# Performance work log

Hardware: AMD Instinct MI355X
Metric: run time of the kernel (lower is better)

## Reference

```python
import jax, jax.numpy as jnp
import numpy as np

H = 8  # num_heads (init kwarg)

def setup_inputs() -> dict:
    key = jax.random.key(0)
    k1, k2, k3, k4 = jax.random.split(key, 4)
    B, S, E = 4, 2048, 512
    x = jax.random.normal(k1, (B, S, E), dtype=jnp.float32)
    # 'normal' keras initializer ~ N(0, 0.05)
    Wq = jax.random.normal(k2, (E, E), dtype=jnp.float32) * 0.05
    Wk = jax.random.normal(k3, (E, E), dtype=jnp.float32) * 0.05
    Wv = jax.random.normal(k4, (E, E), dtype=jnp.float32) * 0.05
    return {"x": x, "Wq": Wq, "Wk": Wk, "Wv": Wv}

def _split_heads(t):
    # [B,S,E] -> [H,B,S,E/H]; matches tf.stack(tf.split(t, H, axis=2))
    B, S, E = t.shape
    return t.reshape(B, S, H, E // H).transpose(2, 0, 1, 3)

def reference(x, Wq, Wk, Wv):
    B, S, E = x.shape
    q = _split_heads(jnp.einsum('bse,ef->bsf', x, Wq))  # [H,B,S,dh]
    k = _split_heads(jnp.einsum('bse,ef->bsf', x, Wk))
    v = _split_heads(jnp.einsum('bse,ef->bsf', x, Wv))
    # NOTE: original has NO 1/sqrt(d) scaling
    scores = jnp.einsum('hbqd,hbkd->hbqk', q, k)         # [H,B,S,S]
    attn = jax.nn.softmax(scores, axis=-1)
    effect = jnp.einsum('hbqk,hbkd->hbqd', attn, v)      # [H,B,S,dh]
    # tf.concat(tf.split(effect, H), axis=-1) + squeeze == merge heads on last dim
    out = effect.transpose(1, 2, 0, 3).reshape(B, S, E)  # [B,S,E]
    return (out, x)
```

## Files before the change

kernel.cpp:

```cpp
#include <hip/hip_runtime.h>

typedef _Float16 f16x8 __attribute__((ext_vector_type(8)));
typedef __fp16 h16x2 __attribute__((ext_vector_type(2)));
typedef float f32x4 __attribute__((ext_vector_type(4)));
typedef float f32x16 __attribute__((ext_vector_type(16)));

#define GF(r) ((((r)&3)) ^ (((r)>>2)&3))
#define LOG2E 1.44269504088896f

#define GLD16(gp, lp) __builtin_amdgcn_global_load_lds( \
    (const __attribute__((address_space(1))) void*)(gp), \
    (__attribute__((address_space(3))) void*)(lp), 16, 0, 0)

__global__ void cvt_all_kernel(const float4* __restrict__ x4, f16x8* __restrict__ xh,
                               const float* __restrict__ Wq, const float* __restrict__ Wk,
                               const float* __restrict__ Wv, _Float16* __restrict__ wt) {
    const int blk = blockIdx.x;
    const int tid = threadIdx.x;
    if (blk < 2048) {
        int i = blk * 256 + tid;
        float4 a = x4[2 * i], b = x4[2 * i + 1];
        f16x8 h;
        h[0] = (_Float16)a.x; h[1] = (_Float16)a.y; h[2] = (_Float16)a.z; h[3] = (_Float16)a.w;
        h[4] = (_Float16)b.x; h[5] = (_Float16)b.y; h[6] = (_Float16)b.z; h[7] = (_Float16)b.w;
        xh[i] = h;
    } else {
        __shared__ _Float16 lt[64 * 66];
        const int t = blk - 2048;
        const int mat = t >> 6, tile = t & 63;
        const int r0 = (tile >> 3) * 64, n0 = (tile & 7) * 64;
        const float* W = (mat == 0) ? Wq : ((mat == 1) ? Wk : Wv);
        const int rr = tid >> 4, c4 = tid & 15;
#pragma unroll
        for (int i = 0; i < 4; ++i) {
            int row = rr + i * 16;
            float4 v = *(const float4*)&W[(size_t)(r0 + row) * 512 + n0 + c4 * 4];
            lt[(c4 * 4 + 0) * 66 + row] = (_Float16)v.x;
            lt[(c4 * 4 + 1) * 66 + row] = (_Float16)v.y;
            lt[(c4 * 4 + 2) * 66 + row] = (_Float16)v.z;
            lt[(c4 * 4 + 3) * 66 + row] = (_Float16)v.w;
        }
        __syncthreads();
        const int nl = tid >> 2, rc = tid & 3;
        _Float16* dst = wt + (size_t)mat * 262144 + (size_t)(n0 + nl) * 512 + r0 + rc * 16;
#pragma unroll
        for (int u = 0; u < 2; ++u)
            *(f16x8*)(dst + u * 8) = *(const f16x8*)&lt[nl * 66 + rc * 16 + u * 8];
    }
}

__global__ __launch_bounds__(256, 3) void gemm_qkv(
    const _Float16* __restrict__ xh, const _Float16* __restrict__ wt,
    _Float16* __restrict__ qh, _Float16* __restrict__ kh, _Float16* __restrict__ vt) {
    __shared__ __align__(16) char gsm[49152];
    const int bid = blockIdx.x;
    const int xcdid = bid & 7, slot = bid >> 3;
    const int mtile = xcdid * 8 + (slot / 12);
    const int rem = slot % 12;
    const int mat = rem >> 2, ntile = rem & 3;
    const _Float16* wp = wt + (size_t)mat * 262144;
    const int tid = threadIdx.x, lane = tid & 63;
    const int g = lane >> 4, c = lane & 15;
    const int wid = tid >> 6, wm = wid >> 1, wn = wid & 1;

    f32x4 acc[4][4];
#pragma unroll
    for (int i = 0; i < 4; ++i)
#pragma unroll
        for (int j = 0; j < 4; ++j) acc[i][j] = (f32x4){0.f, 0.f, 0.f, 0.f};

    const int row0 = tid >> 2, p0 = tid & 3;

    auto GSTAGE = [&](int buf, int ks) {
        _Float16* la_ = (_Float16*)(gsm + buf * 16384);
        _Float16* lb_ = (_Float16*)(gsm + buf * 16384 + 8192);
        int r = row0, pp = p0 ^ GF(r);
        GLD16(xh + (size_t)(mtile * 128 + r) * 512 + ks * 32 + pp * 8, &la_[tid * 8]);
        GLD16(wp + (size_t)(ntile * 128 + r) * 512 + ks * 32 + pp * 8, &lb_[tid * 8]);
        r = 64 + row0; pp = p0 ^ GF(r);
        GLD16(xh + (size_t)(mtile * 128 + r) * 512 + ks * 32 + pp * 8, &la_[(256 + tid) * 8]);
        GLD16(wp + (size_t)(ntile * 128 + r) * 512 + ks * 32 + pp * 8, &lb_[(256 + tid) * 8]);
    };

    auto GTILE = [&](int ks) {
        const _Float16* la = (const _Float16*)(gsm + (ks % 3) * 16384);
        const _Float16* lb = (const _Float16*)(gsm + (ks % 3) * 16384 + 8192);
        f16x8 af[4], bf[4];
#pragma unroll
        for (int i = 0; i < 4; ++i) {
            int ra = wm * 64 + i * 16 + c;
            af[i] = *(const f16x8*)&la[ra * 32 + ((g ^ GF(ra)) * 8)];
            int rb = wn * 64 + i * 16 + c;
            bf[i] = *(const f16x8*)&lb[rb * 32 + ((g ^ GF(rb)) * 8)];
        }
        __builtin_amdgcn_s_setprio(1);
#pragma unroll
        for (int mi = 0; mi < 4; ++mi)
#pragma unroll
            for (int ni = 0; ni < 4; ++ni)
                acc[mi][ni] = __builtin_amdgcn_mfma_f32_16x16x32_f16(af[mi], bf[ni], acc[mi][ni], 0, 0, 0);
        __builtin_amdgcn_s_setprio(0);
    };

    GSTAGE(0, 0); GSTAGE(1, 1);
#pragma unroll 1
    for (int ks = 0; ks < 14; ++ks) {
        asm volatile("s_waitcnt vmcnt(4)" ::: "memory");
        __builtin_amdgcn_s_barrier();
        __builtin_amdgcn_sched_barrier(0);
        GSTAGE((ks + 2) % 3, ks + 2);
        GTILE(ks);
    }
    asm volatile("s_waitcnt vmcnt(4)" ::: "memory");
    __builtin_amdgcn_s_barrier();
    GTILE(14);
    asm volatile("s_waitcnt vmcnt(0)" ::: "memory");
    __builtin_amdgcn_s_barrier();
    GTILE(15);

    __syncthreads();
    _Float16* eb = (_Float16*)gsm + wid * 4608;
    const int rr = lane >> 3, cc = lane & 7;

    if (mat < 2) {
#pragma unroll
        for (int mi = 0; mi < 4; ++mi)
#pragma unroll
            for (int ni = 0; ni < 4; ++ni)
#pragma unroll
                for (int r = 0; r < 4; ++r)
                    eb[(mi * 16 + g * 4 + r) * 72 + ni * 16 + c] = (_Float16)acc[mi][ni][r];
        asm volatile("s_waitcnt lgkmcnt(0)" ::: "memory");
        _Float16* dstm = (mat == 0 ? qh : kh);
#pragma unroll
        for (int p = 0; p < 8; ++p) {
            int row = p * 8 + rr;
            f16x8 v = *(const f16x8*)&eb[row * 72 + cc * 8];
            *(f16x8*)(dstm + (size_t)(mtile * 128 + wm * 64 + row) * 512 +
                      ntile * 128 + wn * 64 + cc * 8) = v;
        }
    } else {
#pragma unroll
        for (int mi = 0; mi < 4; ++mi)
#pragma unroll
            for (int ni = 0; ni < 4; ++ni)
#pragma unroll
                for (int r = 0; r < 4; ++r)
                    eb[(ni * 16 + c) * 72 + mi * 16 + g * 4 + r] = (_Float16)acc[mi][ni][r];
        asm volatile("s_waitcnt lgkmcnt(0)" ::: "memory");
        const int h = ntile * 2 + wn;
        const int mbase = mtile * 128 + wm * 64;
        const int b = mbase >> 11, s0 = mbase & 2047;
#pragma unroll
        for (int p = 0; p < 8; ++p) {
            int d = p * 8 + rr;
            f16x8 v = *(const f16x8*)&eb[d * 72 + cc * 8];
            *(f16x8*)(vt + (((size_t)h * 4 + b) * 64 + d) * 2048 + s0 + cc * 8) = v;
        }
    }
}

__global__ __launch_bounds__(512, 4) void attn_kernel(
    const _Float16* __restrict__ qh, const _Float16* __restrict__ kh,
    const _Float16* __restrict__ vt, const float4* __restrict__ x4,
    float* __restrict__ out) {
    __shared__ __align__(16) char smem[65536];

    const int bid = blockIdx.x;
    const int xcd = bid & 7, idx = bid >> 3;
    const int hb = xcd * 4 + (idx >> 4);
    const int qblk = idx & 15;
    const int h = hb >> 2, b = hb & 3;
    const int tid = threadIdx.x, lane = tid & 63, wid = tid >> 6;
    const int qg = wid & 3, half = wid >> 2;
    const int q = lane & 31, hi = lane >> 5;

    {
        float4* xd = (float4*)(out + 4194304) + (size_t)bid * 2048;
        const float4* xs = x4 + (size_t)bid * 2048;
#pragma unroll
        for (int i = 0; i < 4; ++i) xd[i * 512 + tid] = xs[i * 512 + tid];
    }

    const int qrow0 = qblk * 128 + qg * 32;
    const _Float16* qp = qh + ((size_t)b * 2048 + qrow0) * 512 + h * 64;
    const _Float16* kp = kh + (size_t)b * 2048 * 512 + h * 64;
    const _Float16* vp = vt + (size_t)hb * 64 * 2048;

    const int srow = tid >> 3;
    const int ssw = (tid & 7) ^ ((srow ^ (srow >> 3)) & 7);

    auto STAGE = [&](int i) {
        char* base = smem + (i & 1) * 32768;
        GLD16(kp + ((size_t)(i * 64 + srow) * 512) + ssw * 8, (_Float16*)(base) + tid * 8);
        GLD16(vp + (size_t)srow * 2048 + i * 64 + ssw * 8, (_Float16*)(base + 8192) + tid * 8);
        GLD16(kp + ((size_t)((16 + i) * 64 + srow) * 512) + ssw * 8, (_Float16*)(base + 16384) + tid * 8);
        GLD16(vp + (size_t)srow * 2048 + (16 + i) * 64 + ssw * 8, (_Float16*)(base + 24576) + tid * 8);
    };

    f16x8 aQ[4];
#pragma unroll
    for (int kc = 0; kc < 4; ++kc)
        aQ[kc] = *(const f16x8*)(qp + (size_t)q * 512 + kc * 16 + hi * 8);

    float mrow = -1e30f, lrow = 0.f;
    f32x16 o0, o1;
#pragma unroll
    for (int i = 0; i < 16; ++i) { o0[i] = 0.f; o1[i] = 0.f; }

    const h16x2 ONE2 = {(__fp16)1.0f, (__fp16)1.0f};
    const int swr0 = (q ^ (q >> 3)) & 7;
    const int swr1 = ((32 + q) ^ ((32 + q) >> 3)) & 7;

    auto KPTR = [&](int t) {
        return (const _Float16*)(smem + (t & 1) * 32768 + half * 16384);
    };

    auto QKT2 = [&](const _Float16* kb, f32x16& s0, f32x16& s1) {
        f32x16 z0, z1;
#pragma unroll
        for (int i = 0; i < 16; ++i) { z0[i] = 0.f; z1[i] = 0.f; }
        __builtin_amdgcn_s_setprio(1);
#pragma unroll
        for (int kc = 0; kc < 4; ++kc) {
            f16x8 ak0 = *(const f16x8*)&kb[q * 64 + (((2 * kc + hi) ^ swr0) * 8)];
            f16x8 ak1 = *(const f16x8*)&kb[(32 + q) * 64 + (((2 * kc + hi) ^ swr1) * 8)];
            z0 = __builtin_amdgcn_mfma_f32_32x32x16_f16(ak0, aQ[kc], z0, 0, 0, 0);
            z1 = __builtin_amdgcn_mfma_f32_32x32x16_f16(ak1, aQ[kc], z1, 0, 0, 0);
        }
        __builtin_amdgcn_s_setprio(0);
        s0 = z0; s1 = z1;
    };

    auto SMPV2 = [&](f32x16& s0, f32x16& s1, const _Float16* vb) {
        float pm;
        {
            float m0 = fmaxf(fmaxf(fmaxf(s0[0], s0[1]), s0[2]), s0[3]);
            float m1 = fmaxf(fmaxf(fmaxf(s0[4], s0[5]), s0[6]), s0[7]);
            float m2 = fmaxf(fmaxf(fmaxf(s0[8], s0[9]), s0[10]), s0[11]);
            float m3 = fmaxf(fmaxf(fmaxf(s0[12], s0[13]), s0[14]), s0[15]);
            float m4 = fmaxf(fmaxf(fmaxf(s1[0], s1[1]), s1[2]), s1[3]);
            float m5 = fmaxf(fmaxf(fmaxf(s1[4], s1[5]), s1[6]), s1[7]);
            float m6 = fmaxf(fmaxf(fmaxf(s1[8], s1[9]), s1[10]), s1[11]);
            float m7 = fmaxf(fmaxf(fmaxf(s1[12], s1[13]), s1[14]), s1[15]);
            float t0 = fmaxf(fmaxf(m0, m1), m2);
            float t1 = fmaxf(fmaxf(m3, m4), m5);
            float t2 = fmaxf(m6, m7);
            pm = fmaxf(fmaxf(t0, t1), t2);
        }
        pm = fmaxf(pm, __shfl_xor(pm, 32));
        if (__any(pm > mrow + 8.0f)) {
            const float nm = fmaxf(mrow, pm);
            const float e = __builtin_amdgcn_exp2f((mrow - nm) * LOG2E);
            mrow = nm;
            lrow *= e;
            o0 *= e;
            o1 *= e;
        }
        const float nm2 = mrow * LOG2E;

#pragma unroll
        for (int i = 0; i < 16; ++i)
            s0[i] = __builtin_amdgcn_exp2f(fmaf(s0[i], LOG2E, -nm2));
#pragma unroll
        for (int i = 0; i < 16; ++i)
            s1[i] = __builtin_amdgcn_exp2f(fmaf(s1[i], LOG2E, -nm2));

        f16x8 pf[4];
        float rsA = 0.f, rsB = 0.f;
#pragma unroll
        for (int kb2 = 0; kb2 < 2; ++kb2) {
            const f32x16& sv = kb2 ? s1 : s0;
            h16x2 p0 = __builtin_amdgcn_cvt_pkrtz(sv[0], sv[1]);
            h16x2 p1 = __builtin_amdgcn_cvt_pkrtz(sv[2], sv[3]);
            h16x2 p2 = __builtin_amdgcn_cvt_pkrtz(sv[4], sv[5]);
            h16x2 p3 = __builtin_amdgcn_cvt_pkrtz(sv[6], sv[7]);
            h16x2 p4 = __builtin_amdgcn_cvt_pkrtz(sv[8], sv[9]);
            h16x2 p5 = __builtin_amdgcn_cvt_pkrtz(sv[10], sv[11]);
            h16x2 p6 = __builtin_amdgcn_cvt_pkrtz(sv[12], sv[13]);
            h16x2 p7 = __builtin_amdgcn_cvt_pkrtz(sv[14], sv[15]);
            rsA = __builtin_amdgcn_fdot2(p0, ONE2, rsA, false);
            rsB = __builtin_amdgcn_fdot2(p1, ONE2, rsB, false);
            rsA = __builtin_amdgcn_fdot2(p2, ONE2, rsA, false);
            rsB = __builtin_amdgcn_fdot2(p3, ONE2, rsB, false);
            rsA = __builtin_amdgcn_fdot2(p4, ONE2, rsA, false);
            rsB = __builtin_amdgcn_fdot2(p5, ONE2, rsB, false);
            rsA = __builtin_amdgcn_fdot2(p6, ONE2, rsA, false);
            rsB = __builtin_amdgcn_fdot2(p7, ONE2, rsB, false);
            unsigned t0 = __builtin_bit_cast(unsigned, p0);
            unsigned t1 = __builtin_bit_cast(unsigned, p1);
            unsigned t2 = __builtin_bit_cast(unsigned, p2);
            unsigned t3 = __builtin_bit_cast(unsigned, p3);
            unsigned t4 = __builtin_bit_cast(unsigned, p4);
            unsigned t5 = __builtin_bit_cast(unsigned, p5);
            unsigned t6 = __builtin_bit_cast(unsigned, p6);
            unsigned t7 = __builtin_bit_cast(unsigned, p7);
            asm volatile("v_permlane32_swap_b32 %0, %1" : "+v"(t0), "+v"(t2));
            asm volatile("v_permlane32_swap_b32 %0, %1" : "+v"(t1), "+v"(t3));
            asm volatile("v_permlane32_swap_b32 %0, %1" : "+v"(t4), "+v"(t6));
            asm volatile("v_permlane32_swap_b32 %0, %1" : "+v"(t5), "+v"(t7));
            uint4 u0; u0.x = t0; u0.y = t1; u0.z = t2; u0.w = t3;
            uint4 u1; u1.x = t4; u1.y = t5; u1.z = t6; u1.w = t7;
            pf[2 * kb2 + 0] = __builtin_bit_cast(f16x8, u0);
            pf[2 * kb2 + 1] = __builtin_bit_cast(f16x8, u1);
        }
        lrow += rsA + rsB;

        __builtin_amdgcn_s_setprio(1);
#pragma unroll
        for (int ck = 0; ck < 4; ++ck) {
            f16x8 av0 = *(const f16x8*)&vb[q * 64 + (((2 * ck + hi) ^ swr0) * 8)];
            f16x8 av1 = *(const f16x8*)&vb[(32 + q) * 64 + (((2 * ck + hi) ^ swr1) * 8)];
            o0 = __builtin_amdgcn_mfma_f32_32x32x16_f16(av0, pf[ck], o0, 0, 0, 0);
            o1 = __builtin_amdgcn_mfma_f32_32x32x16_f16(av1, pf[ck], o1, 0, 0, 0);
        }
        __builtin_amdgcn_s_setprio(0);
    };

#define WAITBAR() do { \
    asm volatile("s_waitcnt vmcnt(0)" ::: "memory"); \
    __builtin_amdgcn_s_barrier(); \
    __builtin_amdgcn_sched_barrier(0); \
} while (0)

    f32x16 s0, s1;
    STAGE(0);
    if (half == 0) {
#pragma unroll 1
        for (int t = 0; t < 16; ++t) {
            WAITBAR();
            if (t < 15) STAGE(t + 1);
            QKT2(KPTR(t), s0, s1);
            SMPV2(s0, s1, KPTR(t) + 4096);
        }
    } else {
        WAITBAR();
        STAGE(1);
        QKT2(KPTR(0), s0, s1);
#pragma unroll 1
        for (int t = 1; t < 16; ++t) {
            SMPV2(s0, s1, KPTR(t - 1) + 4096);
            WAITBAR();
            if (t < 15) STAGE(t + 1);
            QKT2(KPTR(t), s0, s1);
        }
        SMPV2(s0, s1, KPTR(15) + 4096);
    }

    lrow += __shfl_xor(lrow, 32);
    __builtin_amdgcn_s_barrier();

    float* xg = (float*)smem + qg * 2112;
    if (half) {
#pragma unroll
        for (int i = 0; i < 16; ++i) {
            xg[i * 64 + lane] = o0[i];
            xg[(16 + i) * 64 + lane] = o1[i];
        }
        if (!hi) { xg[2048 + q] = mrow; xg[2080 + q] = lrow; }
    }
    __syncthreads();
    if (!half) {
        const float m_b = xg[2048 + q], l_b = xg[2080 + q];
        const float m = fmaxf(mrow, m_b);
        const float e_a = __builtin_amdgcn_exp2f((mrow - m) * LOG2E);
        const float e_b = __builtin_amdgcn_exp2f((m_b - m) * LOG2E);
        const float inv = 1.0f / (lrow * e_a + l_b * e_b);
        const float sa = e_a * inv, sb = e_b * inv;
#pragma unroll
        for (int i = 0; i < 16; ++i) {
            o0[i] = o0[i] * sa + xg[i * 64 + lane] * sb;
            o1[i] = o1[i] * sa + xg[(16 + i) * 64 + lane] * sb;
        }
        asm volatile("s_waitcnt lgkmcnt(0)" ::: "memory");
#pragma unroll
        for (int i = 0; i < 16; ++i) {
            int dr = (i & 3) + 8 * (i >> 2) + 4 * hi;
            xg[dr * 33 + q] = o0[i];
            xg[(32 + dr) * 33 + q] = o1[i];
        }
        __builtin_amdgcn_s_waitcnt(0);
        const int d0c = (lane & 15) * 4;
#pragma unroll
        for (int i2 = 0; i2 < 8; ++i2) {
            int qr = 4 * i2 + (lane >> 4);
            float4 v;
            v.x = xg[(d0c + 0) * 33 + qr];
            v.y = xg[(d0c + 1) * 33 + qr];
            v.z = xg[(d0c + 2) * 33 + qr];
            v.w = xg[(d0c + 3) * 33 + qr];
            *(float4*)(out + ((size_t)b * 2048 + qrow0 + qr) * 512 + h * 64 + d0c) = v;
        }
    }
#undef WAITBAR
}

extern "C" void kernel_launch(void* const* d_in, const int* in_sizes, int n_in,
                              void* d_out, int out_size, void* d_ws, size_t ws_size,
                              hipStream_t stream) {
    const float* x = (const float*)d_in[0];
    const float* Wq = (const float*)d_in[1];
    const float* Wk = (const float*)d_in[2];
    const float* Wv = (const float*)d_in[3];
    float* out = (float*)d_out;

    char* ws = (char*)d_ws;
    _Float16* xh = (_Float16*)ws;
    _Float16* wt = (_Float16*)(ws + (size_t)(10u << 20));
    _Float16* qh = (_Float16*)(ws + (size_t)(12u << 20));
    _Float16* kh = (_Float16*)(ws + (size_t)(20u << 20));
    _Float16* vt = (_Float16*)(ws + (size_t)(28u << 20));

    cvt_all_kernel<<<2240, 256, 0, stream>>>((const float4*)x, (f16x8*)xh,
                                             Wq, Wk, Wv, wt);
    gemm_qkv<<<768, 256, 0, stream>>>(xh, wt, qh, kh, vt);
    attn_kernel<<<512, 512, 0, stream>>>(qh, kh, vt, (const float4*)x, out);
}
```

Baseline: 84.48 us.

## Switch attention KV loop to 32-key tiles with 4-stage async pipeline

Restructures the flash-attention inner loop to process 32-key tiles (32 iterations) instead of 64-key tiles, using a 4-deep ring of LDS buffers with partial vmcnt waits so three stages of K/V loads are in flight. It removes the per-iteration full vmcnt(0) drain and the staggered half-specific schedule, aiming to hide global load latency better. In exchange it doubles barrier count and per-tile softmax overhead relative to MFMA work, and it changes the V swizzle layout.

```diff
diff --git a/kernel.cpp b/kernel.cpp
--- a/kernel.cpp
+++ b/kernel.cpp
@@ -187,15 +187,17 @@
     const _Float16* kp = kh + (size_t)b * 2048 * 512 + h * 64;
     const _Float16* vp = vt + (size_t)hb * 64 * 2048;
 
-    const int srow = tid >> 3;
-    const int ssw = (tid & 7) ^ ((srow ^ (srow >> 3)) & 7);
+    const int sHalf = tid >> 8, stt = tid & 255;
+    const int krow = stt >> 3;
+    const int kch = (stt & 7) ^ ((krow ^ (krow >> 3)) & 7);
+    const int vrow = stt >> 2;
+    const int vch = (stt & 3) ^ ((vrow ^ (vrow >> 2)) & 3);
 
     auto STAGE = [&](int i) {
-        char* base = smem + (i & 1) * 32768;
-        GLD16(kp + ((size_t)(i * 64 + srow) * 512) + ssw * 8, (_Float16*)(base) + tid * 8);
-        GLD16(vp + (size_t)srow * 2048 + i * 64 + ssw * 8, (_Float16*)(base + 8192) + tid * 8);
-        GLD16(kp + ((size_t)((16 + i) * 64 + srow) * 512) + ssw * 8, (_Float16*)(base + 16384) + tid * 8);
-        GLD16(vp + (size_t)srow * 2048 + (16 + i) * 64 + ssw * 8, (_Float16*)(base + 24576) + tid * 8);
+        char* base = smem + (i & 3) * 16384 + sHalf * 8192;
+        const int kvt = sHalf * 32 + i;
+        GLD16(kp + ((size_t)(kvt * 32 + krow) * 512) + kch * 8, (_Float16*)base + stt * 8);
+        GLD16(vp + (size_t)vrow * 2048 + kvt * 32 + vch * 8, (_Float16*)(base + 4096) + stt * 8);
     };
 
     f16x8 aQ[4];
@@ -209,44 +211,36 @@
     for (int i = 0; i < 16; ++i) { o0[i] = 0.f; o1[i] = 0.f; }
 
     const h16x2 ONE2 = {(__fp16)1.0f, (__fp16)1.0f};
-    const int swr0 = (q ^ (q >> 3)) & 7;
-    const int swr1 = ((32 + q) ^ ((32 + q) >> 3)) & 7;
-
-    auto KPTR = [&](int t) {
-        return (const _Float16*)(smem + (t & 1) * 32768 + half * 16384);
-    };
-
-    auto QKT2 = [&](const _Float16* kb, f32x16& s0, f32x16& s1) {
-        f32x16 z0, z1;
-#pragma unroll
-        for (int i = 0; i < 16; ++i) { z0[i] = 0.f; z1[i] = 0.f; }
+    const int swk = (q ^ (q >> 3)) & 7;
+    const int swv0 = (q ^ (q >> 2)) & 3;
+    const int swv1 = ((32 + q) ^ ((32 + q) >> 2)) & 3;
+
+    auto TILE = [&](int it) {
+        const _Float16* kb = (const _Float16*)(smem + (it & 3) * 16384 + half * 8192);
+        const _Float16* vb = kb + 2048;
+
+        f32x16 s0;
         __builtin_amdgcn_s_setprio(1);
-#pragma unroll
-        for (int kc = 0; kc < 4; ++kc) {
-            f16x8 ak0 = *(const f16x8*)&kb[q * 64 + (((2 * kc + hi) ^ swr0) * 8)];
-            f16x8 ak1 = *(const f16x8*)&kb[(32 + q) * 64 + (((2 * kc + hi) ^ swr1) * 8)];
-            z0 = __builtin_amdgcn_mfma_f32_32x32x16_f16(ak0, aQ[kc], z0, 0, 0, 0);
-            z1 = __builtin_amdgcn_mfma_f32_32x32x16_f16(ak1, aQ[kc], z1, 0, 0, 0);
+        {
+            f32x16 z;
+#pragma unroll
+            for (int i = 0; i < 16; ++i) z[i] = 0.f;
+#pragma unroll
+            for (int kc = 0; kc < 4; ++kc) {
+                f16x8 ak = *(const f16x8*)&kb[q * 64 + (((2 * kc + hi) ^ swk) * 8)];
+                z = __builtin_amdgcn_mfma_f32_32x32x16_f16(ak, aQ[kc], z, 0, 0, 0);
+            }
+            s0 = z;
         }
         __builtin_amdgcn_s_setprio(0);
-        s0 = z0; s1 = z1;
-    };
-
-    auto SMPV2 = [&](f32x16& s0, f32x16& s1, const _Float16* vb) {
+
         float pm;
         {
             float m0 = fmaxf(fmaxf(fmaxf(s0[0], s0[1]), s0[2]), s0[3]);
             float m1 = fmaxf(fmaxf(fmaxf(s0[4], s0[5]), s0[6]), s0[7]);
             float m2 = fmaxf(fmaxf(fmaxf(s0[8], s0[9]), s0[10]), s0[11]);
             float m3 = fmaxf(fmaxf(fmaxf(s0[12], s0[13]), s0[14]), s0[15]);
-            float m4 = fmaxf(fmaxf(fmaxf(s1[0], s1[1]), s1[2]), s1[3]);
-            float m5 = fmaxf(fmaxf(fmaxf(s1[4], s1[5]), s1[6]), s1[7]);
-            float m6 = fmaxf(fmaxf(fmaxf(s1[8], s1[9]), s1[10]), s1[11]);
-            float m7 = fmaxf(fmaxf(fmaxf(s1[12], s1[13]), s1[14]), s1[15]);
-            float t0 = fmaxf(fmaxf(m0, m1), m2);
-            float t1 = fmaxf(fmaxf(m3, m4), m5);
-            float t2 = fmaxf(m6, m7);
-            pm = fmaxf(fmaxf(t0, t1), t2);
+            pm = fmaxf(fmaxf(m0, m1), fmaxf(m2, m3));
         }
         pm = fmaxf(pm, __shfl_xor(pm, 32));
         if (__any(pm > mrow + 8.0f)) {
@@ -262,23 +256,18 @@
 #pragma unroll
         for (int i = 0; i < 16; ++i)
             s0[i] = __builtin_amdgcn_exp2f(fmaf(s0[i], LOG2E, -nm2));
-#pragma unroll
-        for (int i = 0; i < 16; ++i)
-            s1[i] = __builtin_amdgcn_exp2f(fmaf(s1[i], LOG2E, -nm2));
-
-        f16x8 pf[4];
+
+        f16x8 pf[2];
         float rsA = 0.f, rsB = 0.f;
-#pragma unroll
-        for (int kb2 = 0; kb2 < 2; ++kb2) {
-            const f32x16& sv = kb2 ? s1 : s0;
-            h16x2 p0 = __builtin_amdgcn_cvt_pkrtz(sv[0], sv[1]);
-            h16x2 p1 = __builtin_amdgcn_cvt_pkrtz(sv[2], sv[3]);
-            h16x2 p2 = __builtin_amdgcn_cvt_pkrtz(sv[4], sv[5]);
-            h16x2 p3 = __builtin_amdgcn_cvt_pkrtz(sv[6], sv[7]);
-            h16x2 p4 = __builtin_amdgcn_cvt_pkrtz(sv[8], sv[9]);
-            h16x2 p5 = __builtin_amdgcn_cvt_pkrtz(sv[10], sv[11]);
-            h16x2 p6 = __builtin_amdgcn_cvt_pkrtz(sv[12], sv[13]);
-            h16x2 p7 = __builtin_amdgcn_cvt_pkrtz(sv[14], sv[15]);
+        {
+            h16x2 p0 = __builtin_amdgcn_cvt_pkrtz(s0[0], s0[1]);
+            h16x2 p1 = __builtin_amdgcn_cvt_pkrtz(s0[2], s0[3]);
+            h16x2 p2 = __builtin_amdgcn_cvt_pkrtz(s0[4], s0[5]);
+            h16x2 p3 = __builtin_amdgcn_cvt_pkrtz(s0[6], s0[7]);
+            h16x2 p4 = __builtin_amdgcn_cvt_pkrtz(s0[8], s0[9]);
+            h16x2 p5 = __builtin_amdgcn_cvt_pkrtz(s0[10], s0[11]);
+            h16x2 p6 = __builtin_amdgcn_cvt_pkrtz(s0[12], s0[13]);
+            h16x2 p7 = __builtin_amdgcn_cvt_pkrtz(s0[14], s0[15]);
             rsA = __builtin_amdgcn_fdot2(p0, ONE2, rsA, false);
             rsB = __builtin_amdgcn_fdot2(p1, ONE2, rsB, false);
             rsA = __builtin_amdgcn_fdot2(p2, ONE2, rsA, false);
@@ -301,51 +290,39 @@
             asm volatile("v_permlane32_swap_b32 %0, %1" : "+v"(t5), "+v"(t7));
             uint4 u0; u0.x = t0; u0.y = t1; u0.z = t2; u0.w = t3;
             uint4 u1; u1.x = t4; u1.y = t5; u1.z = t6; u1.w = t7;
-            pf[2 * kb2 + 0] = __builtin_bit_cast(f16x8, u0);
-            pf[2 * kb2 + 1] = __builtin_bit_cast(f16x8, u1);
+            pf[0] = __builtin_bit_cast(f16x8, u0);
+            pf[1] = __builtin_bit_cast(f16x8, u1);
         }
         lrow += rsA + rsB;
 
         __builtin_amdgcn_s_setprio(1);
 #pragma unroll
-        for (int ck = 0; ck < 4; ++ck) {
-            f16x8 av0 = *(const f16x8*)&vb[q * 64 + (((2 * ck + hi) ^ swr0) * 8)];
-            f16x8 av1 = *(const f16x8*)&vb[(32 + q) * 64 + (((2 * ck + hi) ^ swr1) * 8)];
+        for (int ck = 0; ck < 2; ++ck) {
+            f16x8 av0 = *(const f16x8*)&vb[q * 32 + (((2 * ck + hi) ^ swv0) * 8)];
+            f16x8 av1 = *(const f16x8*)&vb[(32 + q) * 32 + (((2 * ck + hi) ^ swv1) * 8)];
             o0 = __builtin_amdgcn_mfma_f32_32x32x16_f16(av0, pf[ck], o0, 0, 0, 0);
             o1 = __builtin_amdgcn_mfma_f32_32x32x16_f16(av1, pf[ck], o1, 0, 0, 0);
         }
         __builtin_amdgcn_s_setprio(0);
     };
 
-#define WAITBAR() do { \
-    asm volatile("s_waitcnt vmcnt(0)" ::: "memory"); \
-    __builtin_amdgcn_s_barrier(); \
-    __builtin_amdgcn_sched_barrier(0); \
-} while (0)
-
-    f32x16 s0, s1;
-    STAGE(0);
-    if (half == 0) {
+    STAGE(0); STAGE(1); STAGE(2);
 #pragma unroll 1
-        for (int t = 0; t < 16; ++t) {
-            WAITBAR();
-            if (t < 15) STAGE(t + 1);
-            QKT2(KPTR(t), s0, s1);
-            SMPV2(s0, s1, KPTR(t) + 4096);
-        }
-    } else {
-        WAITBAR();
-        STAGE(1);
-        QKT2(KPTR(0), s0, s1);
-#pragma unroll 1
-        for (int t = 1; t < 16; ++t) {
-            SMPV2(s0, s1, KPTR(t - 1) + 4096);
-            WAITBAR();
-            if (t < 15) STAGE(t + 1);
-            QKT2(KPTR(t), s0, s1);
-        }
-        SMPV2(s0, s1, KPTR(15) + 4096);
-    }
+    for (int t = 0; t < 30; ++t) {
+        asm volatile("s_waitcnt vmcnt(8)" ::: "memory");
+        __builtin_amdgcn_s_barrier();
+        __builtin_amdgcn_sched_barrier(0);
+        STAGE(t + 3);
+        TILE(t);
+    }
+    asm volatile("s_waitcnt vmcnt(4)" ::: "memory");
+    __builtin_amdgcn_s_barrier();
+    __builtin_amdgcn_sched_barrier(0);
+    TILE(30);
+    asm volatile("s_waitcnt vmcnt(0)" ::: "memory");
+    __builtin_amdgcn_s_barrier();
+    __builtin_amdgcn_sched_barrier(0);
+    TILE(31);
 
     lrow += __shfl_xor(lrow, 32);
     __builtin_amdgcn_s_barrier();
@@ -392,7 +369,6 @@
             *(float4*)(out + ((size_t)b * 2048 + qrow0 + qr) * 512 + h * 64 + d0c) = v;
         }
     }
-#undef WAITBAR
 }
 
 extern "C" void kernel_launch(void* const* d_in, const int* in_sizes, int n_in,
```

Result: no change. 86.09 us (+1.9%).
